# Kernel optimization log

Measured on AMD Instinct MI355X. Metric: run time of the kernel, lower is better.

## Reference

```python
import jax, jax.numpy as jnp
import numpy as np

N_NODES = 50000
N_EDGES = 800000
D_FEAT = 128
D_EDGE = 64
N_HEADS = 4
OUT_DIM = 32
HID = N_HEADS * OUT_DIM  # 128


def segment_softmax(logits, seg, num_segments):
    # jraph.segment_softmax: subtract per-segment max, exp, normalize by per-segment sum
    seg_max = jax.ops.segment_max(logits, seg, num_segments=num_segments)
    e = jnp.exp(logits - seg_max[seg])
    denom = jax.ops.segment_sum(e, seg, num_segments=num_segments)
    return e / denom[seg]


def setup_inputs() -> dict:
    key = jax.random.key(0)
    ks = jax.random.split(key, 12)
    s = 1.0 / np.sqrt(D_FEAT)
    se = 1.0 / np.sqrt(D_EDGE)
    return {
        "nodes": jax.random.normal(ks[0], (N_NODES, D_FEAT), jnp.float32),
        "edges": jax.random.normal(ks[1], (N_EDGES, D_EDGE), jnp.float32),
        "senders": jax.random.randint(ks[2], (N_EDGES,), 0, N_NODES, jnp.int32),
        "receivers": jax.random.randint(ks[3], (N_EDGES,), 0, N_NODES, jnp.int32),
        "Wq": jax.random.normal(ks[4], (D_FEAT, HID), jnp.float32) * s,
        "bq": jnp.zeros((HID,), jnp.float32),
        "Wk": jax.random.normal(ks[5], (D_FEAT, HID), jnp.float32) * s,
        "bk": jnp.zeros((HID,), jnp.float32),
        "Wv": jax.random.normal(ks[6], (D_FEAT, HID), jnp.float32) * s,
        "bv": jnp.zeros((HID,), jnp.float32),
        "We": jax.random.normal(ks[7], (D_EDGE, HID), jnp.float32) * se,
        "Wu": jax.random.normal(ks[8], (D_FEAT, OUT_DIM), jnp.float32) * s,
        "bu": jnp.zeros((OUT_DIM,), jnp.float32),
    }


def reference(nodes, edges, senders, receivers, Wq, bq, Wk, bk, Wv, bv, We, Wu, bu):
    n_nodes = nodes.shape[0]
    send_feats = nodes[senders]    # [E, D]
    recv_feats = nodes[receivers]  # [E, D]

    q = (recv_feats @ Wq + bq).reshape(-1, N_HEADS, OUT_DIM)
    k = (send_feats @ Wk + bk).reshape(-1, N_HEADS, OUT_DIM)
    v = (send_feats @ Wv + bv).reshape(-1, N_HEADS, OUT_DIM)
    e = (edges @ We).reshape(-1, N_HEADS, OUT_DIM)

    attn = (q * k).sum(-1) / jnp.sqrt(jnp.asarray(OUT_DIM, q.dtype))  # [E, H]
    attn = segment_softmax(attn, receivers, n_nodes)                  # [E, H]

    msgs = (attn[:, :, None] * (v + e)).mean(axis=1)                  # [E, OUT_DIM]
    aggr = jax.ops.segment_sum(msgs, receivers, num_segments=n_nodes) # [N, OUT_DIM]

    feats = nodes @ Wu + bu
    return jax.nn.relu(feats + aggr)
```

## Files before the change

kernel.cpp:

```cpp
#include <hip/hip_runtime.h>
#include <math.h>

#define N_NODES 50000
#define N_EDGES 800000
#define D_FEAT 128
#define D_EDGE 64
#define HID 128
#define OUT_DIM 32

typedef unsigned short u16;
typedef short bf16x8 __attribute__((ext_vector_type(8)));
typedef float f32x4 __attribute__((ext_vector_type(4)));

__device__ __forceinline__ u16 f2bf(float x) {
    unsigned u = __float_as_uint(x);
    unsigned r = (u >> 16) & 1u;
    return (u16)((u + 0x7FFFu + r) >> 16);
}
__device__ __forceinline__ float bf2f(u16 s) { return __uint_as_float(((unsigned)s) << 16); }
__device__ __forceinline__ float bflo(unsigned u) { return __uint_as_float(u << 16); }
__device__ __forceinline__ float bfhi(unsigned u) { return __uint_as_float(u & 0xFFFF0000u); }

__global__ void zero_i32(int* __restrict__ p, int n) {
    int i = blockIdx.x * 256 + threadIdx.x;
    if (i < n) p[i] = 0;
}

__global__ void prep_weights(const float* __restrict__ Wq, const float* __restrict__ Wk,
                             const float* __restrict__ Wv, const float* __restrict__ We,
                             u16* __restrict__ WT_all, u16* __restrict__ WeTg) {
    int id = blockIdx.x * 256 + threadIdx.x;
    if (id < 49152) {
        int m = id >> 14, rem = id & 16383;
        int c = rem >> 7, k = rem & 127;
        const float* W = (m == 0) ? Wq : (m == 1) ? Wk : Wv;
        WT_all[id] = f2bf(W[k * HID + c]);
    } else {
        int j = id - 49152;
        int c = j >> 6, k = j & 63;
        WeTg[j] = f2bf(We[k * HID + c]);
    }
}

__global__ __launch_bounds__(256) void node_qkv_mfma(
    const float* __restrict__ nodes, const u16* __restrict__ WT_all,
    const float* __restrict__ bq, const float* __restrict__ bk, const float* __restrict__ bv,
    u16* __restrict__ Q, u16* __restrict__ Kk, u16* __restrict__ Vp)
{
    const int mtile = blockIdx.y;
    const int n0 = blockIdx.x * 128;
    const u16* WT = WT_all + (size_t)mtile * 16384;
    const float* bvec = (mtile == 0) ? bq : (mtile == 1) ? bk : bv;
    u16* C = (mtile == 0) ? Q : (mtile == 1) ? Kk : Vp;

    __shared__ __align__(16) u16 Alds[128 * 136];

    const int tid = threadIdx.x;
    #pragma unroll
    for (int it = 0; it < 16; ++it) {
        int idx = tid + it * 256;
        int row = idx >> 5, k4 = (idx & 31) * 4;
        float4 v = make_float4(0.f, 0.f, 0.f, 0.f);
        if (n0 + row < N_NODES)
            v = *(const float4*)&nodes[(size_t)(n0 + row) * D_FEAT + k4];
        ushort4 b;
        b.x = f2bf(v.x); b.y = f2bf(v.y); b.z = f2bf(v.z); b.w = f2bf(v.w);
        *(ushort4*)&Alds[row * 136 + k4] = b;
    }
    __syncthreads();

    const int wave = tid >> 6, lane = tid & 63;
    const int quad = lane >> 4, l15 = lane & 15;
    const int eb = wave * 32;

    bf16x8 afr[2][4];
    #pragma unroll
    for (int rt = 0; rt < 2; ++rt)
        #pragma unroll
        for (int ks = 0; ks < 4; ++ks)
            afr[rt][ks] = *(const bf16x8*)&Alds[(eb + rt * 16 + l15) * 136 + ks * 32 + quad * 8];

    f32x4 acc[2][8];
    #pragma unroll
    for (int rt = 0; rt < 2; ++rt)
        #pragma unroll
        for (int ct = 0; ct < 8; ++ct)
            acc[rt][ct] = (f32x4){0.f, 0.f, 0.f, 0.f};

    #pragma unroll
    for (int ks = 0; ks < 4; ++ks) {
        #pragma unroll
        for (int ct = 0; ct < 8; ++ct) {
            bf16x8 b = *(const bf16x8*)&WT[(ct * 16 + l15) * 128 + ks * 32 + quad * 8];
            acc[0][ct] = __builtin_amdgcn_mfma_f32_16x16x32_bf16(afr[0][ks], b, acc[0][ct], 0, 0, 0);
            acc[1][ct] = __builtin_amdgcn_mfma_f32_16x16x32_bf16(afr[1][ks], b, acc[1][ct], 0, 0, 0);
        }
    }

    #pragma unroll
    for (int ct = 0; ct < 8; ++ct) {
        int cbase = ct * 16 + l15;
        float bias = bvec[cbase];
        int oidx = (mtile == 2) ? ((cbase & 31) * 4 + (cbase >> 5)) : cbase;
        #pragma unroll
        for (int rt = 0; rt < 2; ++rt)
            #pragma unroll
            for (int r = 0; r < 4; ++r) {
                int n = n0 + eb + rt * 16 + quad * 4 + r;
                if (n < N_NODES)
                    C[(size_t)n * HID + oidx] = f2bf(acc[rt][ct][r] + bias);
            }
    }
}

__global__ void hist_kernel(const int* __restrict__ receivers, int* __restrict__ count) {
    int e = blockIdx.x * 256 + threadIdx.x;
    atomicAdd(&count[receivers[e]], 1);
}

__global__ __launch_bounds__(256) void scan1(const int* __restrict__ count,
                                             int* __restrict__ incl, int* __restrict__ bsum) {
    __shared__ int sh[256];
    int gid = blockIdx.x * 256 + threadIdx.x;
    int v = (gid < N_NODES) ? count[gid] : 0;
    sh[threadIdx.x] = v; __syncthreads();
    #pragma unroll
    for (int off = 1; off < 256; off <<= 1) {
        int t = (threadIdx.x >= off) ? sh[threadIdx.x - off] : 0;
        __syncthreads();
        sh[threadIdx.x] += t;
        __syncthreads();
    }
    if (gid < N_NODES) incl[gid] = sh[threadIdx.x];
    if (threadIdx.x == 255) bsum[blockIdx.x] = sh[255];
}

__global__ __launch_bounds__(256) void scan2(const int* __restrict__ bsum,
                                             int* __restrict__ boff, int nblocks) {
    __shared__ int sh[256];
    int v = (threadIdx.x < nblocks) ? bsum[threadIdx.x] : 0;
    sh[threadIdx.x] = v; __syncthreads();
    #pragma unroll
    for (int off = 1; off < 256; off <<= 1) {
        int t = (threadIdx.x >= off) ? sh[threadIdx.x - off] : 0;
        __syncthreads();
        sh[threadIdx.x] += t;
        __syncthreads();
    }
    boff[threadIdx.x] = sh[threadIdx.x] - v;
}

__global__ __launch_bounds__(256) void scan3(const int* __restrict__ incl,
                                             const int* __restrict__ count,
                                             const int* __restrict__ boff,
                                             int* __restrict__ startp, int* __restrict__ cursor) {
    int gid = blockIdx.x * 256 + threadIdx.x;
    if (gid < N_NODES) {
        int ex = incl[gid] - count[gid] + boff[blockIdx.x];
        startp[gid] = ex;
        cursor[gid] = ex;
    }
    if (gid == 0) startp[N_NODES] = N_EDGES;
}

__global__ void scatter_kernel(const int* __restrict__ receivers,
                               int* __restrict__ cursor, int* __restrict__ sorted,
                               int* __restrict__ epos) {
    int e = blockIdx.x * 256 + threadIdx.x;
    int r = receivers[e];
    int pos = atomicAdd(&cursor[r], 1);
    sorted[pos] = e;
    epos[e] = pos;
}

__global__ __launch_bounds__(256) void edge_logits_v2(
    const u16* __restrict__ Q, const u16* __restrict__ K,
    const int* __restrict__ senders, const int* __restrict__ receivers,
    const int* __restrict__ sorted, float* __restrict__ wbuf)
{
    int id = blockIdx.x * 256 + threadIdx.x;
    int i = id >> 1, half = id & 1;
    int e = sorted[i];
    int s = senders[e], r = receivers[e];
    const uint4* qp = (const uint4*)&Q[(size_t)r * HID + half * 64];
    const uint4* kp = (const uint4*)&K[(size_t)s * HID + half * 64];
    float a0 = 0.f, a1 = 0.f;
    #pragma unroll
    for (int j = 0; j < 4; ++j) {
        uint4 a = qp[j], b = kp[j];
        a0 += bflo(a.x) * bflo(b.x) + bfhi(a.x) * bfhi(b.x);
        a0 += bflo(a.y) * bflo(b.y) + bfhi(a.y) * bfhi(b.y);
        a0 += bflo(a.z) * bflo(b.z) + bfhi(a.z) * bfhi(b.z);
        a0 += bflo(a.w) * bflo(b.w) + bfhi(a.w) * bfhi(b.w);
    }
    #pragma unroll
    for (int j = 4; j < 8; ++j) {
        uint4 a = qp[j], b = kp[j];
        a1 += bflo(a.x) * bflo(b.x) + bfhi(a.x) * bfhi(b.x);
        a1 += bflo(a.y) * bflo(b.y) + bfhi(a.y) * bfhi(b.y);
        a1 += bflo(a.z) * bflo(b.z) + bfhi(a.z) * bfhi(b.z);
        a1 += bflo(a.w) * bflo(b.w) + bfhi(a.w) * bfhi(b.w);
    }
    const float sc = 0.17677669529663687f;
    float2 o = make_float2(expf(a0 * sc), expf(a1 * sc));
    *(float2*)&wbuf[(size_t)i * 4 + half * 2] = o;
}

__global__ __launch_bounds__(256) void denom_norm2(
    const int* __restrict__ startp, float* __restrict__ wbuf)
{
    int n = blockIdx.x * 256 + threadIdx.x;
    if (n >= N_NODES) return;
    int s = startp[n], e = startp[n + 1];
    float4 a = make_float4(0.f, 0.f, 0.f, 0.f);
    for (int i = s; i < e; ++i) {
        float4 w = *(const float4*)&wbuf[(size_t)i * 4];
        a.x += w.x; a.y += w.y; a.z += w.z; a.w += w.w;
    }
    float4 inv;
    inv.x = 0.25f / a.x; inv.y = 0.25f / a.y; inv.z = 0.25f / a.z; inv.w = 0.25f / a.w;
    for (int i = s; i < e; ++i) {
        float4 w = *(const float4*)&wbuf[(size_t)i * 4];
        w.x *= inv.x; w.y *= inv.y; w.z *= inv.z; w.w *= inv.w;
        *(float4*)&wbuf[(size_t)i * 4] = w;
    }
}

__global__ __launch_bounds__(256) void edge_messages_v6(
    const float* __restrict__ edges, const u16* __restrict__ WeTg,
    const u16* __restrict__ Vp, const float* __restrict__ wbuf,
    const int* __restrict__ senders, const int* __restrict__ epos,
    u16* __restrict__ msg)
{
    __shared__ __align__(16) u16 Ae[128 * 72];

    const int tid = threadIdx.x;
    const int e0 = blockIdx.x * 128;
    const int wave = tid >> 6, lane = tid & 63;
    const int quad = lane >> 4, l15 = lane & 15;
    const int eb = wave * 32;

    int snd8[8], pos8[8];
    #pragma unroll
    for (int idx = 0; idx < 8; ++idx) {
        int el = e0 + eb + (idx >> 2) * 16 + quad * 4 + (idx & 3);
        snd8[idx] = senders[el];
        pos8[idx] = epos[el];
    }
    float w8[8][4];
    #pragma unroll
    for (int idx = 0; idx < 8; ++idx) {
        float4 w = *(const float4*)&wbuf[(size_t)pos8[idx] * 4];
        w8[idx][0] = w.x; w8[idx][1] = w.y; w8[idx][2] = w.z; w8[idx][3] = w.w;
    }

    #pragma unroll
    for (int it = 0; it < 8; ++it) {
        int idx = tid + it * 256;
        int e  = idx >> 4;
        int k4 = (idx & 15) * 4;
        float4 v = *(const float4*)&edges[(size_t)(e0 + e) * D_EDGE + k4];
        ushort4 b;
        b.x = f2bf(v.x); b.y = f2bf(v.y); b.z = f2bf(v.z); b.w = f2bf(v.w);
        *(ushort4*)&Ae[e * 72 + k4] = b;
    }
    __syncthreads();

    bf16x8 afr[2][2];
    #pragma unroll
    for (int rt = 0; rt < 2; ++rt)
        #pragma unroll
        for (int ks = 0; ks < 2; ++ks)
            afr[rt][ks] = *(const bf16x8*)&Ae[(eb + rt * 16 + l15) * 72 + ks * 32 + quad * 8];

    #pragma unroll
    for (int p = 0; p < 2; ++p) {
        const int d = p * 16 + l15;
        ushort4 vp8[8];
        #pragma unroll
        for (int idx = 0; idx < 8; ++idx)
            vp8[idx] = *(const ushort4*)&Vp[(size_t)snd8[idx] * HID + d * 4];

        f32x4 acc[2][4];
        #pragma unroll
        for (int rt = 0; rt < 2; ++rt)
            #pragma unroll
            for (int c = 0; c < 4; ++c)
                acc[rt][c] = (f32x4){0.f, 0.f, 0.f, 0.f};

        #pragma unroll
        for (int ks = 0; ks < 2; ++ks) {
            #pragma unroll
            for (int c = 0; c < 4; ++c) {
                bf16x8 b = *(const bf16x8*)&WeTg[((2 * c + p) * 16 + l15) * 64 + ks * 32 + quad * 8];
                acc[0][c] = __builtin_amdgcn_mfma_f32_16x16x32_bf16(afr[0][ks], b, acc[0][c], 0, 0, 0);
                acc[1][c] = __builtin_amdgcn_mfma_f32_16x16x32_bf16(afr[1][ks], b, acc[1][c], 0, 0, 0);
            }
        }

        #pragma unroll
        for (int idx = 0; idx < 8; ++idx) {
            int rt = idx >> 2, r = idx & 3;
            float out = w8[idx][0] * (acc[rt][0][r] + bf2f(vp8[idx].x))
                      + w8[idx][1] * (acc[rt][1][r] + bf2f(vp8[idx].y))
                      + w8[idx][2] * (acc[rt][2][r] + bf2f(vp8[idx].z))
                      + w8[idx][3] * (acc[rt][3][r] + bf2f(vp8[idx].w));
            msg[(size_t)pos8[idx] * OUT_DIM + d] = f2bf(out);
        }
    }
}

__global__ __launch_bounds__(256) void aggregate3(
    const u16* __restrict__ msg, const float* __restrict__ nodes,
    const float* __restrict__ Wu, const float* __restrict__ bu,
    const int* __restrict__ startp, float* __restrict__ out)
{
    int id = blockIdx.x * 256 + threadIdx.x;
    int n = id >> 5, d = id & 31;
    float acc = bu[d];
    #pragma unroll 4
    for (int i = 0; i < D_FEAT; ++i)
        acc += nodes[(size_t)n * D_FEAT + i] * Wu[i * OUT_DIM + d];
    int s = startp[n], e = startp[n + 1];
    for (int i = s; i < e; ++i)
        acc += bf2f(msg[(size_t)i * OUT_DIM + d]);
    out[id] = fmaxf(acc, 0.f);
}

extern "C" void kernel_launch(void* const* d_in, const int* in_sizes, int n_in,
                              void* d_out, int out_size, void* d_ws, size_t ws_size,
                              hipStream_t stream) {
    const float* nodes     = (const float*)d_in[0];
    const float* edges     = (const float*)d_in[1];
    const int*   senders   = (const int*)d_in[2];
    const int*   receivers = (const int*)d_in[3];
    const float* Wq = (const float*)d_in[4];
    const float* bq = (const float*)d_in[5];
    const float* Wk = (const float*)d_in[6];
    const float* bk = (const float*)d_in[7];
    const float* Wv = (const float*)d_in[8];
    const float* bv = (const float*)d_in[9];
    const float* We = (const float*)d_in[10];
    const float* Wu = (const float*)d_in[11];
    const float* bu = (const float*)d_in[12];
    float* out = (float*)d_out;

    char* p = (char*)d_ws;
    u16* Qb    = (u16*)p; p += (size_t)N_NODES * HID * 2;
    u16* Kb    = (u16*)p; p += (size_t)N_NODES * HID * 2;
    u16* Vperm = (u16*)p; p += (size_t)N_NODES * HID * 2;
    u16* WT_all= (u16*)p; p += (size_t)3 * HID * HID * 2;
    u16* WeTg  = (u16*)p; p += (size_t)HID * D_EDGE * 2;
    float* wbuf = (float*)p; p += (size_t)N_EDGES * 4 * 4;
    u16* msg   = (u16*)p; p += (size_t)N_EDGES * OUT_DIM * 2;
    int* count  = (int*)p; p += (size_t)N_NODES * 4;
    int* incl   = (int*)p; p += (size_t)N_NODES * 4;
    int* startp = (int*)p; p += (size_t)(N_NODES + 4) * 4;
    int* cursor = (int*)p; p += (size_t)N_NODES * 4;
    int* sorted = (int*)p; p += (size_t)N_EDGES * 4;
    int* epos   = (int*)p; p += (size_t)N_EDGES * 4;
    int* bsum   = (int*)p; p += 256 * 4;
    int* boff   = (int*)p; p += 256 * 4;

    const int SCAN_BLOCKS = (N_NODES + 255) / 256;

    hipLaunchKernelGGL(zero_i32, dim3(SCAN_BLOCKS), dim3(256), 0, stream, count, N_NODES);
    hipLaunchKernelGGL(hist_kernel, dim3(N_EDGES / 256), dim3(256), 0, stream,
                       receivers, count);
    hipLaunchKernelGGL(scan1, dim3(SCAN_BLOCKS), dim3(256), 0, stream, count, incl, bsum);
    hipLaunchKernelGGL(scan2, dim3(1), dim3(256), 0, stream, bsum, boff, SCAN_BLOCKS);
    hipLaunchKernelGGL(scan3, dim3(SCAN_BLOCKS), dim3(256), 0, stream,
                       incl, count, boff, startp, cursor);
    hipLaunchKernelGGL(scatter_kernel, dim3(N_EDGES / 256), dim3(256), 0, stream,
                       receivers, cursor, sorted, epos);
    hipLaunchKernelGGL(prep_weights, dim3(57344 / 256), dim3(256), 0, stream,
                       Wq, Wk, Wv, We, WT_all, WeTg);
    hipLaunchKernelGGL(node_qkv_mfma, dim3((N_NODES + 127) / 128, 3), dim3(256), 0, stream,
                       nodes, WT_all, bq, bk, bv, Qb, Kb, Vperm);
    hipLaunchKernelGGL(edge_logits_v2, dim3(N_EDGES * 2 / 256), dim3(256), 0, stream,
                       Qb, Kb, senders, receivers, sorted, wbuf);
    hipLaunchKernelGGL(denom_norm2, dim3(SCAN_BLOCKS), dim3(256), 0, stream,
                       startp, wbuf);
    hipLaunchKernelGGL(edge_messages_v6, dim3(N_EDGES / 128), dim3(256), 0, stream,
                       edges, WeTg, Vperm, wbuf, senders, epos, msg);
    hipLaunchKernelGGL(aggregate3, dim3(N_NODES * OUT_DIM / 256), dim3(256), 0, stream,
                       msg, nodes, Wu, bu, startp, out);
}
```

Baseline: 680.8 us.

## Fuse QKV projections, pre-sort edge indices, split softmax normalization into inverse pass

The QKV projection now runs once per 128-node tile and loops over all three weight matrices, so the node features are loaded and converted to bf16 once instead of three times. Each wave stages its own LDS slice, which removes the block-wide barrier. The scatter step now writes sender and receiver ids already in sorted order, dropping the indirect lookup through the sorted edge list in the logits kernel. The softmax denominator kernel uses four lanes per node and writes only per-node inverse sums, with normalization applied on the fly in the message kernel. This avoids a second read-modify-write pass over wbuf, at the cost of an extra gather of receivers and inverses per edge.

```diff
diff --git a/kernel.cpp b/kernel.cpp
--- a/kernel.cpp
+++ b/kernel.cpp
@@ -42,74 +42,75 @@
     }
 }
 
-__global__ __launch_bounds__(256) void node_qkv_mfma(
+__global__ __launch_bounds__(256) void node_qkv_v2(
     const float* __restrict__ nodes, const u16* __restrict__ WT_all,
     const float* __restrict__ bq, const float* __restrict__ bk, const float* __restrict__ bv,
     u16* __restrict__ Q, u16* __restrict__ Kk, u16* __restrict__ Vp)
 {
-    const int mtile = blockIdx.y;
-    const int n0 = blockIdx.x * 128;
-    const u16* WT = WT_all + (size_t)mtile * 16384;
-    const float* bvec = (mtile == 0) ? bq : (mtile == 1) ? bk : bv;
-    u16* C = (mtile == 0) ? Q : (mtile == 1) ? Kk : Vp;
-
-    __shared__ __align__(16) u16 Alds[128 * 136];
+    __shared__ __align__(16) u16 Alds[4][32 * 136];
 
     const int tid = threadIdx.x;
+    const int wave = tid >> 6, lane = tid & 63;
+    const int quad = lane >> 4, l15 = lane & 15;
+    const int rowbase = blockIdx.x * 128 + wave * 32;
+
+    u16* As = &Alds[wave][0];
     #pragma unroll
     for (int it = 0; it < 16; ++it) {
-        int idx = tid + it * 256;
+        int idx = lane + it * 64;
         int row = idx >> 5, k4 = (idx & 31) * 4;
         float4 v = make_float4(0.f, 0.f, 0.f, 0.f);
-        if (n0 + row < N_NODES)
-            v = *(const float4*)&nodes[(size_t)(n0 + row) * D_FEAT + k4];
+        if (rowbase + row < N_NODES)
+            v = *(const float4*)&nodes[(size_t)(rowbase + row) * D_FEAT + k4];
         ushort4 b;
         b.x = f2bf(v.x); b.y = f2bf(v.y); b.z = f2bf(v.z); b.w = f2bf(v.w);
-        *(ushort4*)&Alds[row * 136 + k4] = b;
-    }
-    __syncthreads();
-
-    const int wave = tid >> 6, lane = tid & 63;
-    const int quad = lane >> 4, l15 = lane & 15;
-    const int eb = wave * 32;
+        *(ushort4*)&As[row * 136 + k4] = b;
+    }
 
     bf16x8 afr[2][4];
     #pragma unroll
     for (int rt = 0; rt < 2; ++rt)
         #pragma unroll
         for (int ks = 0; ks < 4; ++ks)
-            afr[rt][ks] = *(const bf16x8*)&Alds[(eb + rt * 16 + l15) * 136 + ks * 32 + quad * 8];
-
-    f32x4 acc[2][8];
-    #pragma unroll
-    for (int rt = 0; rt < 2; ++rt)
-        #pragma unroll
-        for (int ct = 0; ct < 8; ++ct)
-            acc[rt][ct] = (f32x4){0.f, 0.f, 0.f, 0.f};
-
-    #pragma unroll
-    for (int ks = 0; ks < 4; ++ks) {
+            afr[rt][ks] = *(const bf16x8*)&As[(rt * 16 + l15) * 136 + ks * 32 + quad * 8];
+
+    #pragma unroll
+    for (int m = 0; m < 3; ++m) {
+        const u16* WT = WT_all + (size_t)m * 16384;
+        const float* bvec = (m == 0) ? bq : (m == 1) ? bk : bv;
+        u16* C = (m == 0) ? Q : (m == 1) ? Kk : Vp;
+
+        f32x4 acc[2][8];
+        #pragma unroll
+        for (int rt = 0; rt < 2; ++rt)
+            #pragma unroll
+            for (int ct = 0; ct < 8; ++ct)
+                acc[rt][ct] = (f32x4){0.f, 0.f, 0.f, 0.f};
+
+        #pragma unroll
+        for (int ks = 0; ks < 4; ++ks) {
+            #pragma unroll
+            for (int ct = 0; ct < 8; ++ct) {
+                bf16x8 b = *(const bf16x8*)&WT[(ct * 16 + l15) * 128 + ks * 32 + quad * 8];
+                acc[0][ct] = __builtin_amdgcn_mfma_f32_16x16x32_bf16(afr[0][ks], b, acc[0][ct], 0, 0, 0);
+                acc[1][ct] = __builtin_amdgcn_mfma_f32_16x16x32_bf16(afr[1][ks], b, acc[1][ct], 0, 0, 0);
+            }
+        }
+
         #pragma unroll
         for (int ct = 0; ct < 8; ++ct) {
-            bf16x8 b = *(const bf16x8*)&WT[(ct * 16 + l15) * 128 + ks * 32 + quad * 8];
-            acc[0][ct] = __builtin_amdgcn_mfma_f32_16x16x32_bf16(afr[0][ks], b, acc[0][ct], 0, 0, 0);
-            acc[1][ct] = __builtin_amdgcn_mfma_f32_16x16x32_bf16(afr[1][ks], b, acc[1][ct], 0, 0, 0);
+            int cbase = ct * 16 + l15;
+            float bias = bvec[cbase];
+            int oidx = (m == 2) ? ((cbase & 31) * 4 + (cbase >> 5)) : cbase;
+            #pragma unroll
+            for (int rt = 0; rt < 2; ++rt)
+                #pragma unroll
+                for (int r = 0; r < 4; ++r) {
+                    int n = rowbase + rt * 16 + quad * 4 + r;
+                    if (n < N_NODES)
+                        C[(size_t)n * HID + oidx] = f2bf(acc[rt][ct][r] + bias);
+                }
         }
-    }
-
-    #pragma unroll
-    for (int ct = 0; ct < 8; ++ct) {
-        int cbase = ct * 16 + l15;
-        float bias = bvec[cbase];
-        int oidx = (mtile == 2) ? ((cbase & 31) * 4 + (cbase >> 5)) : cbase;
-        #pragma unroll
-        for (int rt = 0; rt < 2; ++rt)
-            #pragma unroll
-            for (int r = 0; r < 4; ++r) {
-                int n = n0 + eb + rt * 16 + quad * 4 + r;
-                if (n < N_NODES)
-                    C[(size_t)n * HID + oidx] = f2bf(acc[rt][ct][r] + bias);
-            }
     }
 }
 
@@ -163,25 +164,26 @@
     if (gid == 0) startp[N_NODES] = N_EDGES;
 }
 
-__global__ void scatter_kernel(const int* __restrict__ receivers,
-                               int* __restrict__ cursor, int* __restrict__ sorted,
-                               int* __restrict__ epos) {
+__global__ void scatter_v2(const int* __restrict__ senders, const int* __restrict__ receivers,
+                           int* __restrict__ cursor, int* __restrict__ epos,
+                           int* __restrict__ ssend, int* __restrict__ srecv) {
     int e = blockIdx.x * 256 + threadIdx.x;
     int r = receivers[e];
+    int s = senders[e];
     int pos = atomicAdd(&cursor[r], 1);
-    sorted[pos] = e;
     epos[e] = pos;
-}
-
-__global__ __launch_bounds__(256) void edge_logits_v2(
+    ssend[pos] = s;
+    srecv[pos] = r;
+}
+
+__global__ __launch_bounds__(256) void edge_logits_v3(
     const u16* __restrict__ Q, const u16* __restrict__ K,
-    const int* __restrict__ senders, const int* __restrict__ receivers,
-    const int* __restrict__ sorted, float* __restrict__ wbuf)
+    const int* __restrict__ ssend, const int* __restrict__ srecv,
+    float* __restrict__ wbuf)
 {
     int id = blockIdx.x * 256 + threadIdx.x;
     int i = id >> 1, half = id & 1;
-    int e = sorted[i];
-    int s = senders[e], r = receivers[e];
+    int s = ssend[i], r = srecv[i];
     const uint4* qp = (const uint4*)&Q[(size_t)r * HID + half * 64];
     const uint4* kp = (const uint4*)&K[(size_t)s * HID + half * 64];
     float a0 = 0.f, a1 = 0.f;
@@ -206,72 +208,78 @@
     *(float2*)&wbuf[(size_t)i * 4 + half * 2] = o;
 }
 
-__global__ __launch_bounds__(256) void denom_norm2(
-    const int* __restrict__ startp, float* __restrict__ wbuf)
-{
-    int n = blockIdx.x * 256 + threadIdx.x;
+__global__ __launch_bounds__(256) void denom_inv(
+    const int* __restrict__ startp, const float* __restrict__ wbuf,
+    float* __restrict__ inv4)
+{
+    int id = blockIdx.x * 256 + threadIdx.x;
+    int n = id >> 2, j = id & 3;
     if (n >= N_NODES) return;
     int s = startp[n], e = startp[n + 1];
     float4 a = make_float4(0.f, 0.f, 0.f, 0.f);
-    for (int i = s; i < e; ++i) {
+    for (int i = s + j; i < e; i += 4) {
         float4 w = *(const float4*)&wbuf[(size_t)i * 4];
         a.x += w.x; a.y += w.y; a.z += w.z; a.w += w.w;
     }
-    float4 inv;
-    inv.x = 0.25f / a.x; inv.y = 0.25f / a.y; inv.z = 0.25f / a.z; inv.w = 0.25f / a.w;
-    for (int i = s; i < e; ++i) {
-        float4 w = *(const float4*)&wbuf[(size_t)i * 4];
-        w.x *= inv.x; w.y *= inv.y; w.z *= inv.z; w.w *= inv.w;
-        *(float4*)&wbuf[(size_t)i * 4] = w;
-    }
-}
-
-__global__ __launch_bounds__(256) void edge_messages_v6(
+    #pragma unroll
+    for (int off = 1; off < 4; off <<= 1) {
+        a.x += __shfl_xor(a.x, off);
+        a.y += __shfl_xor(a.y, off);
+        a.z += __shfl_xor(a.z, off);
+        a.w += __shfl_xor(a.w, off);
+    }
+    if (j == 0) {
+        float4 iv;
+        iv.x = 0.25f / a.x; iv.y = 0.25f / a.y; iv.z = 0.25f / a.z; iv.w = 0.25f / a.w;
+        *(float4*)&inv4[(size_t)n * 4] = iv;
+    }
+}
+
+__global__ __launch_bounds__(256) void edge_messages_v7(
     const float* __restrict__ edges, const u16* __restrict__ WeTg,
     const u16* __restrict__ Vp, const float* __restrict__ wbuf,
-    const int* __restrict__ senders, const int* __restrict__ epos,
+    const int* __restrict__ senders, const int* __restrict__ receivers,
+    const int* __restrict__ epos, const float* __restrict__ inv4,
     u16* __restrict__ msg)
 {
-    __shared__ __align__(16) u16 Ae[128 * 72];
+    __shared__ __align__(16) u16 Ae[4][32 * 72];
 
     const int tid = threadIdx.x;
-    const int e0 = blockIdx.x * 128;
     const int wave = tid >> 6, lane = tid & 63;
     const int quad = lane >> 4, l15 = lane & 15;
-    const int eb = wave * 32;
+    const int e0w = blockIdx.x * 128 + wave * 32;
 
     int snd8[8], pos8[8];
+    float w8[8][4];
     #pragma unroll
     for (int idx = 0; idx < 8; ++idx) {
-        int el = e0 + eb + (idx >> 2) * 16 + quad * 4 + (idx & 3);
+        int el = e0w + (idx >> 2) * 16 + quad * 4 + (idx & 3);
         snd8[idx] = senders[el];
         pos8[idx] = epos[el];
-    }
-    float w8[8][4];
-    #pragma unroll
-    for (int idx = 0; idx < 8; ++idx) {
-        float4 w = *(const float4*)&wbuf[(size_t)pos8[idx] * 4];
-        w8[idx][0] = w.x; w8[idx][1] = w.y; w8[idx][2] = w.z; w8[idx][3] = w.w;
-    }
-
+        int r = receivers[el];
+        float4 w  = *(const float4*)&wbuf[(size_t)pos8[idx] * 4];
+        float4 iv = *(const float4*)&inv4[(size_t)r * 4];
+        w8[idx][0] = w.x * iv.x; w8[idx][1] = w.y * iv.y;
+        w8[idx][2] = w.z * iv.z; w8[idx][3] = w.w * iv.w;
+    }
+
+    u16* As = &Ae[wave][0];
     #pragma unroll
     for (int it = 0; it < 8; ++it) {
-        int idx = tid + it * 256;
-        int e  = idx >> 4;
-        int k4 = (idx & 15) * 4;
-        float4 v = *(const float4*)&edges[(size_t)(e0 + e) * D_EDGE + k4];
+        int idx = lane + it * 64;
+        int row = idx >> 4, k4 = (idx & 15) * 4;
+        float4 v = *(const float4*)&edges[(size_t)(e0w + row) * D_EDGE + k4];
         ushort4 b;
         b.x = f2bf(v.x); b.y = f2bf(v.y); b.z = f2bf(v.z); b.w = f2bf(v.w);
-        *(ushort4*)&Ae[e * 72 + k4] = b;
-    }
-    __syncthreads();
+        *(ushort4*)&As[row * 72 + k4] = b;
+    }
 
     bf16x8 afr[2][2];
     #pragma unroll
     for (int rt = 0; rt < 2; ++rt)
         #pragma unroll
         for (int ks = 0; ks < 2; ++ks)
-            afr[rt][ks] = *(const bf16x8*)&Ae[(eb + rt * 16 + l15) * 72 + ks * 32 + quad * 8];
+            afr[rt][ks] = *(const bf16x8*)&As[(rt * 16 + l15) * 72 + ks * 32 + quad * 8];
 
     #pragma unroll
     for (int p = 0; p < 2; ++p) {
@@ -353,12 +361,14 @@
     u16* WeTg  = (u16*)p; p += (size_t)HID * D_EDGE * 2;
     float* wbuf = (float*)p; p += (size_t)N_EDGES * 4 * 4;
     u16* msg   = (u16*)p; p += (size_t)N_EDGES * OUT_DIM * 2;
+    float* inv4 = (float*)p; p += (size_t)N_NODES * 4 * 4;
     int* count  = (int*)p; p += (size_t)N_NODES * 4;
     int* incl   = (int*)p; p += (size_t)N_NODES * 4;
     int* startp = (int*)p; p += (size_t)(N_NODES + 4) * 4;
     int* cursor = (int*)p; p += (size_t)N_NODES * 4;
-    int* sorted = (int*)p; p += (size_t)N_EDGES * 4;
     int* epos   = (int*)p; p += (size_t)N_EDGES * 4;
+    int* ssend  = (int*)p; p += (size_t)N_EDGES * 4;
+    int* srecv  = (int*)p; p += (size_t)N_EDGES * 4;
     int* bsum   = (int*)p; p += 256 * 4;
     int* boff   = (int*)p; p += 256 * 4;
 
@@ -371,18 +381,18 @@
     hipLaunchKernelGGL(scan2, dim3(1), dim3(256), 0, stream, bsum, boff, SCAN_BLOCKS);
     hipLaunchKernelGGL(scan3, dim3(SCAN_BLOCKS), dim3(256), 0, stream,
                        incl, count, boff, startp, cursor);
-    hipLaunchKernelGGL(scatter_kernel, dim3(N_EDGES / 256), dim3(256), 0, stream,
-                       receivers, cursor, sorted, epos);
+    hipLaunchKernelGGL(scatter_v2, dim3(N_EDGES / 256), dim3(256), 0, stream,
+                       senders, receivers, cursor, epos, ssend, srecv);
     hipLaunchKernelGGL(prep_weights, dim3(57344 / 256), dim3(256), 0, stream,
                        Wq, Wk, Wv, We, WT_all, WeTg);
-    hipLaunchKernelGGL(node_qkv_mfma, dim3((N_NODES + 127) / 128, 3), dim3(256), 0, stream,
+    hipLaunchKernelGGL(node_qkv_v2, dim3((N_NODES + 127) / 128), dim3(256), 0, stream,
                        nodes, WT_all, bq, bk, bv, Qb, Kb, Vperm);
-    hipLaunchKernelGGL(edge_logits_v2, dim3(N_EDGES * 2 / 256), dim3(256), 0, stream,
-                       Qb, Kb, senders, receivers, sorted, wbuf);
-    hipLaunchKernelGGL(denom_norm2, dim3(SCAN_BLOCKS), dim3(256), 0, stream,
-                       startp, wbuf);
-    hipLaunchKernelGGL(edge_messages_v6, dim3(N_EDGES / 128), dim3(256), 0, stream,
-                       edges, WeTg, Vperm, wbuf, senders, epos, msg);
+    hipLaunchKernelGGL(edge_logits_v3, dim3(N_EDGES * 2 / 256), dim3(256), 0, stream,
+                       Qb, Kb, ssend, srecv, wbuf);
+    hipLaunchKernelGGL(denom_inv, dim3((N_NODES * 4 + 255) / 256), dim3(256), 0, stream,
+                       startp, wbuf, inv4);
+    hipLaunchKernelGGL(edge_messages_v7, dim3(N_EDGES / 128), dim3(256), 0, stream,
+                       edges, WeTg, Vperm, wbuf, senders, receivers, epos, inv4, msg);
     hipLaunchKernelGGL(aggregate3, dim3(N_NODES * OUT_DIM / 256), dim3(256), 0, stream,
                        msg, nodes, Wu, bu, startp, out);
 }
```

After: 668.8 us. About the same (-1.8%).
